# Kernel tuning notes

Measured on AMD Instinct MI355X. Metric: run time of the kernel, lower is better.

Reference implementation:

```python
import jax, jax.numpy as jnp
import numpy as np

N_USERS = 100000
EMBED_DIM = 64
MAX_NEIGHBORS = 50
BATCH = 16384


def setup_inputs() -> dict:
    key = jax.random.key(0)
    k1, k2, k3, k4 = jax.random.split(key, 4)
    nodes = jax.random.randint(k1, (BATCH,), 0, N_USERS, dtype=jnp.int64 if jax.config.read('jax_enable_x64') else jnp.int32)
    u_u = jax.random.randint(k2, (N_USERS, MAX_NEIGHBORS), 0, N_USERS, dtype=nodes.dtype)
    # integer-valued degrees in [0, MAX_NEIGHBORS], zeros included to exercise the inf-mask
    u_u_l = jax.random.randint(k3, (N_USERS, 1), 0, MAX_NEIGHBORS + 1).astype(jnp.float32)
    emb = jax.random.normal(k4, (N_USERS, EMBED_DIM), dtype=jnp.float32)
    return {"nodes": nodes, "u_u": u_u, "u_u_l": u_u_l, "emb": emb}


def reference(nodes, u_u, u_u_l, emb):
    tem_adj = u_u[nodes]                    # [B, K] neighbor ids
    e_u = emb[tem_adj]                      # [B, K, D] gathered neighbor embeddings
    N_a = u_u_l[nodes]                      # [B, 1] degree of center node
    N_b = u_u_l[tem_adj][..., 0]            # [B, K] degree of neighbors
    att_w = 1.0 / (jnp.sqrt(N_a) * jnp.sqrt(N_b))  # [B, K]
    att_w = jnp.where(jnp.isinf(att_w), 0.0, att_w)
    # bmm(e_u^T [B,D,K], att_w [B,K,1]) -> [B,D]
    embed_matrix = jnp.einsum('bkd,bk->bd', e_u, att_w)
    return embed_matrix
```

## Files before the change

### kernel.cpp

```cpp
#include <hip/hip_runtime.h>

#define D 64
#define K 50
#define GROUPS 8
#define KPAD 56
#define ITERS (KPAD / GROUPS)
#define RPB 8
#define THREADS 256

__global__ __launch_bounds__(THREADS)
void prep_q8(const float* __restrict__ emb, const float* __restrict__ deg,
             unsigned* __restrict__ emb8, float* __restrict__ rtab,
             float* __restrict__ wtab, int nuser)
{
    const int tid = blockIdx.x * THREADS + threadIdx.x;
    const int row = tid >> 4;
    const int sub = tid & 15;
    if (row >= nuser) return;

    const float4 f = ((const float4*)emb)[row * 16 + sub];
    float m = fmaxf(fmaxf(fabsf(f.x), fabsf(f.y)), fmaxf(fabsf(f.z), fabsf(f.w)));
    #pragma unroll
    for (int off = 1; off < 16; off <<= 1)
        m = fmaxf(m, __shfl_xor(m, off));
    const float inv = (m > 0.0f) ? 127.0f / m : 0.0f;
    const int q0 = (int)rintf(f.x * inv);
    const int q1 = (int)rintf(f.y * inv);
    const int q2 = (int)rintf(f.z * inv);
    const int q3 = (int)rintf(f.w * inv);
    const unsigned pk = (q0 & 0xFF) | ((q1 & 0xFF) << 8) |
                        ((q2 & 0xFF) << 16) | ((unsigned)(q3 & 0xFF) << 24);
    emb8[row * 16 + sub] = pk;
    if (sub == 0) {
        const float n = deg[row];
        const float r = (n > 0.0f) ? rsqrtf(n) : 0.0f;
        rtab[row] = r;
        wtab[row] = r * m * (1.0f / 127.0f);
    }
}

__device__ __forceinline__ float sb(unsigned v, int byte) {
    return (float)((int)(v << (24 - 8 * byte)) >> 24);
}

__global__ __launch_bounds__(THREADS)
void social_agg_q8(const int* __restrict__ nodes,
                   const int* __restrict__ u_u,
                   const float* __restrict__ rtab,
                   const float* __restrict__ wtab,
                   const unsigned* __restrict__ emb8,
                   float* __restrict__ out,
                   int batch)
{
    __shared__ uint2 nw[RPB][KPAD];
    const int base = blockIdx.x * RPB;

    for (int p = threadIdx.x; p < RPB * KPAD; p += THREADS) {
        const int r   = p / KPAD;
        const int k   = p - r * KPAD;
        const int row = base + r;
        int nb = 0; float w = 0.0f;
        if (row < batch && k < K) {
            const int node = nodes[row];
            nb = u_u[node * K + k];
            w  = rtab[node] * wtab[nb];
        }
        nw[r][k] = make_uint2((unsigned)nb, __float_as_uint(w));
    }
    __syncthreads();

    const int wave = threadIdx.x >> 6;
    const int lane = threadIdx.x & 63;
    const int g    = lane >> 3;
    const int sub  = lane & 7;
    const int r0   = wave * 2;
    const int row0 = base + r0;

    float a0[8] = {0,0,0,0,0,0,0,0};
    float a1[8] = {0,0,0,0,0,0,0,0};
    #pragma unroll
    for (int i = 0; i < ITERS; ++i) {
        const uint2 e0 = nw[r0][i * GROUPS + g];
        const uint2 e1 = nw[r0 + 1][i * GROUPS + g];
        const float w0 = __uint_as_float(e0.y);
        const float w1 = __uint_as_float(e1.y);
        const uint2 v0 = *(const uint2*)(emb8 + (size_t)e0.x * (D / 4) + sub * 2);
        const uint2 v1 = *(const uint2*)(emb8 + (size_t)e1.x * (D / 4) + sub * 2);
        a0[0] += w0 * sb(v0.x, 0); a0[1] += w0 * sb(v0.x, 1);
        a0[2] += w0 * sb(v0.x, 2); a0[3] += w0 * sb(v0.x, 3);
        a0[4] += w0 * sb(v0.y, 0); a0[5] += w0 * sb(v0.y, 1);
        a0[6] += w0 * sb(v0.y, 2); a0[7] += w0 * sb(v0.y, 3);
        a1[0] += w1 * sb(v1.x, 0); a1[1] += w1 * sb(v1.x, 1);
        a1[2] += w1 * sb(v1.x, 2); a1[3] += w1 * sb(v1.x, 3);
        a1[4] += w1 * sb(v1.y, 0); a1[5] += w1 * sb(v1.y, 1);
        a1[6] += w1 * sb(v1.y, 2); a1[7] += w1 * sb(v1.y, 3);
    }

    #pragma unroll
    for (int off = 8; off <= 32; off <<= 1) {
        #pragma unroll
        for (int j = 0; j < 8; ++j) { a0[j] += __shfl_xor(a0[j], off);
                                      a1[j] += __shfl_xor(a1[j], off); }
    }

    if (g == 0) {
        if (row0 < batch) {
            float* o = out + (size_t)row0 * D + sub * 8;
            *(float4*)(o)     = make_float4(a0[0], a0[1], a0[2], a0[3]);
            *(float4*)(o + 4) = make_float4(a0[4], a0[5], a0[6], a0[7]);
        }
        if (row0 + 1 < batch) {
            float* o = out + (size_t)(row0 + 1) * D + sub * 8;
            *(float4*)(o)     = make_float4(a1[0], a1[1], a1[2], a1[3]);
            *(float4*)(o + 4) = make_float4(a1[4], a1[5], a1[6], a1[7]);
        }
    }
}

__global__ __launch_bounds__(THREADS)
void social_agg_f32(const int* __restrict__ nodes,
                    const int* __restrict__ u_u,
                    const float* __restrict__ u_u_l,
                    const float* __restrict__ emb,
                    float* __restrict__ out,
                    int batch)
{
    __shared__ uint2 nw[4][52];
    const int base = blockIdx.x * 4;
    const int p = threadIdx.x;
    if (p < 4 * 52) {
        const int r = p / 52, k = p - r * 52, row = base + r;
        int nb = 0; float w = 0.0f;
        if (row < batch && k < K) {
            const int node = nodes[row];
            const float Na = u_u_l[node];
            nb = u_u[node * K + k];
            const float prod = Na * u_u_l[nb];
            w = (prod > 0.0f) ? rsqrtf(prod) : 0.0f;
        }
        nw[r][k] = make_uint2((unsigned)nb, __float_as_uint(w));
    }
    __syncthreads();
    const int wave = threadIdx.x >> 6, lane = threadIdx.x & 63;
    const int kk = lane >> 4, sub = lane & 15, row = base + wave;
    float4 acc = make_float4(0.f, 0.f, 0.f, 0.f);
    #pragma unroll
    for (int i = 0; i < 13; ++i) {
        const uint2 e = nw[wave][i * 4 + kk];
        const float wk = __uint_as_float(e.y);
        const float4 v = *(const float4*)(emb + (size_t)e.x * D + sub * 4);
        acc.x += wk * v.x; acc.y += wk * v.y; acc.z += wk * v.z; acc.w += wk * v.w;
    }
    #pragma unroll
    for (int off = 16; off <= 32; off <<= 1) {
        acc.x += __shfl_xor(acc.x, off);
        acc.y += __shfl_xor(acc.y, off);
        acc.z += __shfl_xor(acc.z, off);
        acc.w += __shfl_xor(acc.w, off);
    }
    if (row < batch && kk == 0)
        *(float4*)(out + (size_t)row * D + sub * 4) = acc;
}

extern "C" void kernel_launch(void* const* d_in, const int* in_sizes, int n_in,
                              void* d_out, int out_size, void* d_ws, size_t ws_size,
                              hipStream_t stream) {
    const int*   nodes = (const int*)d_in[0];
    const int*   u_u   = (const int*)d_in[1];
    const float* u_u_l = (const float*)d_in[2];
    const float* emb   = (const float*)d_in[3];
    float*       out   = (float*)d_out;

    const int batch = in_sizes[0];
    const int nuser = in_sizes[1] / K;

    const size_t emb8_bytes = (size_t)nuser * D;
    const size_t tab_bytes  = (size_t)nuser * 4;
    if (ws_size >= emb8_bytes + 2 * tab_bytes) {
        unsigned* emb8 = (unsigned*)d_ws;
        float*    rtab = (float*)((char*)d_ws + emb8_bytes);
        float*    wtab = (float*)((char*)d_ws + emb8_bytes + tab_bytes);
        const int pthreads = nuser * 16;
        const int pblocks  = (pthreads + THREADS - 1) / THREADS;
        prep_q8<<<pblocks, THREADS, 0, stream>>>(emb, u_u_l, emb8, rtab, wtab, nuser);
        const int blocks = (batch + RPB - 1) / RPB;
        social_agg_q8<<<blocks, THREADS, 0, stream>>>(nodes, u_u, rtab, wtab, emb8,
                                                      out, batch);
    } else {
        const int blocks = (batch + 3) / 4;
        social_agg_f32<<<blocks, THREADS, 0, stream>>>(nodes, u_u, u_u_l, emb,
                                                       out, batch);
    }
}
```

Before: 29.24 us.

## Interleave per-neighbor scale into quantized embedding rows, apply center factor at output

Each quantized embedding row now carries its per-row scale (neighbor rsqrt degree times quantization scale) in a padded 72-byte record. The main kernel reads the scale together with the int8 payload instead of doing a separate random gather into wtab during the staging phase. The center-node rsqrt factor is applied once per output row. Padding slots point to a zeroed sentinel row. This removes one dependent random gather per neighbor, but the row stride is no longer aligned to 64 bytes, so some rows span two cache lines.

```diff
diff --git a/kernel.cpp b/kernel.cpp
--- a/kernel.cpp
+++ b/kernel.cpp
@@ -7,15 +7,19 @@
 #define ITERS (KPAD / GROUPS)
 #define RPB 8
 #define THREADS 256
+#define ROW_BYTES 72
 
 __global__ __launch_bounds__(THREADS)
 void prep_q8(const float* __restrict__ emb, const float* __restrict__ deg,
-             unsigned* __restrict__ emb8, float* __restrict__ rtab,
-             float* __restrict__ wtab, int nuser)
+             char* __restrict__ tab, float* __restrict__ rtab, int nuser)
 {
     const int tid = blockIdx.x * THREADS + threadIdx.x;
     const int row = tid >> 4;
     const int sub = tid & 15;
+
+    if (blockIdx.x == 0 && threadIdx.x < ROW_BYTES / 4)
+        ((unsigned*)(tab + (size_t)nuser * ROW_BYTES))[threadIdx.x] = 0u;
+
     if (row >= nuser) return;
 
     const float4 f = ((const float4*)emb)[row * 16 + sub];
@@ -30,12 +34,13 @@
     const int q3 = (int)rintf(f.w * inv);
     const unsigned pk = (q0 & 0xFF) | ((q1 & 0xFF) << 8) |
                         ((q2 & 0xFF) << 16) | ((unsigned)(q3 & 0xFF) << 24);
-    emb8[row * 16 + sub] = pk;
+    char* rbase = tab + (size_t)row * ROW_BYTES;
+    *(unsigned*)(rbase + sub * 4) = pk;
     if (sub == 0) {
         const float n = deg[row];
         const float r = (n > 0.0f) ? rsqrtf(n) : 0.0f;
         rtab[row] = r;
-        wtab[row] = r * m * (1.0f / 127.0f);
+        *(float*)(rbase + 64) = r * m * (1.0f / 127.0f);
     }
 }
 
@@ -47,25 +52,26 @@
 void social_agg_q8(const int* __restrict__ nodes,
                    const int* __restrict__ u_u,
                    const float* __restrict__ rtab,
-                   const float* __restrict__ wtab,
-                   const unsigned* __restrict__ emb8,
+                   const char* __restrict__ tab,
                    float* __restrict__ out,
-                   int batch)
+                   int batch, int nuser)
 {
-    __shared__ uint2 nw[RPB][KPAD];
+    __shared__ unsigned ids[RPB][KPAD];
+    __shared__ float    cfac[RPB];
     const int base = blockIdx.x * RPB;
 
     for (int p = threadIdx.x; p < RPB * KPAD; p += THREADS) {
         const int r   = p / KPAD;
         const int k   = p - r * KPAD;
         const int row = base + r;
-        int nb = 0; float w = 0.0f;
-        if (row < batch && k < K) {
-            const int node = nodes[row];
-            nb = u_u[node * K + k];
-            w  = rtab[node] * wtab[nb];
-        }
-        nw[r][k] = make_uint2((unsigned)nb, __float_as_uint(w));
+        unsigned nb = (unsigned)nuser;
+        if (row < batch && k < K)
+            nb = (unsigned)u_u[nodes[row] * K + k];
+        ids[r][k] = nb;
+    }
+    if (threadIdx.x < RPB) {
+        const int row = base + threadIdx.x;
+        cfac[threadIdx.x] = (row < batch) ? rtab[nodes[row]] : 0.0f;
     }
     __syncthreads();
 
@@ -80,20 +86,22 @@
     float a1[8] = {0,0,0,0,0,0,0,0};
     #pragma unroll
     for (int i = 0; i < ITERS; ++i) {
-        const uint2 e0 = nw[r0][i * GROUPS + g];
-        const uint2 e1 = nw[r0 + 1][i * GROUPS + g];
-        const float w0 = __uint_as_float(e0.y);
-        const float w1 = __uint_as_float(e1.y);
-        const uint2 v0 = *(const uint2*)(emb8 + (size_t)e0.x * (D / 4) + sub * 2);
-        const uint2 v1 = *(const uint2*)(emb8 + (size_t)e1.x * (D / 4) + sub * 2);
-        a0[0] += w0 * sb(v0.x, 0); a0[1] += w0 * sb(v0.x, 1);
-        a0[2] += w0 * sb(v0.x, 2); a0[3] += w0 * sb(v0.x, 3);
-        a0[4] += w0 * sb(v0.y, 0); a0[5] += w0 * sb(v0.y, 1);
-        a0[6] += w0 * sb(v0.y, 2); a0[7] += w0 * sb(v0.y, 3);
-        a1[0] += w1 * sb(v1.x, 0); a1[1] += w1 * sb(v1.x, 1);
-        a1[2] += w1 * sb(v1.x, 2); a1[3] += w1 * sb(v1.x, 3);
-        a1[4] += w1 * sb(v1.y, 0); a1[5] += w1 * sb(v1.y, 1);
-        a1[6] += w1 * sb(v1.y, 2); a1[7] += w1 * sb(v1.y, 3);
+        const unsigned nb0 = ids[r0][i * GROUPS + g];
+        const unsigned nb1 = ids[r0 + 1][i * GROUPS + g];
+        const char* b0 = tab + (size_t)nb0 * ROW_BYTES;
+        const char* b1 = tab + (size_t)nb1 * ROW_BYTES;
+        const uint2 v0 = *(const uint2*)(b0 + sub * 8);
+        const uint2 v1 = *(const uint2*)(b1 + sub * 8);
+        const float f0 = *(const float*)(b0 + 64);
+        const float f1 = *(const float*)(b1 + 64);
+        a0[0] += f0 * sb(v0.x, 0); a0[1] += f0 * sb(v0.x, 1);
+        a0[2] += f0 * sb(v0.x, 2); a0[3] += f0 * sb(v0.x, 3);
+        a0[4] += f0 * sb(v0.y, 0); a0[5] += f0 * sb(v0.y, 1);
+        a0[6] += f0 * sb(v0.y, 2); a0[7] += f0 * sb(v0.y, 3);
+        a1[0] += f1 * sb(v1.x, 0); a1[1] += f1 * sb(v1.x, 1);
+        a1[2] += f1 * sb(v1.x, 2); a1[3] += f1 * sb(v1.x, 3);
+        a1[4] += f1 * sb(v1.y, 0); a1[5] += f1 * sb(v1.y, 1);
+        a1[6] += f1 * sb(v1.y, 2); a1[7] += f1 * sb(v1.y, 3);
     }
 
     #pragma unroll
@@ -105,14 +113,16 @@
 
     if (g == 0) {
         if (row0 < batch) {
+            const float c = cfac[r0];
             float* o = out + (size_t)row0 * D + sub * 8;
-            *(float4*)(o)     = make_float4(a0[0], a0[1], a0[2], a0[3]);
-            *(float4*)(o + 4) = make_float4(a0[4], a0[5], a0[6], a0[7]);
+            *(float4*)(o)     = make_float4(c*a0[0], c*a0[1], c*a0[2], c*a0[3]);
+            *(float4*)(o + 4) = make_float4(c*a0[4], c*a0[5], c*a0[6], c*a0[7]);
         }
         if (row0 + 1 < batch) {
+            const float c = cfac[r0 + 1];
             float* o = out + (size_t)(row0 + 1) * D + sub * 8;
-            *(float4*)(o)     = make_float4(a1[0], a1[1], a1[2], a1[3]);
-            *(float4*)(o + 4) = make_float4(a1[4], a1[5], a1[6], a1[7]);
+            *(float4*)(o)     = make_float4(c*a1[0], c*a1[1], c*a1[2], c*a1[3]);
+            *(float4*)(o + 4) = make_float4(c*a1[4], c*a1[5], c*a1[6], c*a1[7]);
         }
     }
 }
@@ -174,18 +184,17 @@
     const int batch = in_sizes[0];
     const int nuser = in_sizes[1] / K;
 
-    const size_t emb8_bytes = (size_t)nuser * D;
-    const size_t tab_bytes  = (size_t)nuser * 4;
-    if (ws_size >= emb8_bytes + 2 * tab_bytes) {
-        unsigned* emb8 = (unsigned*)d_ws;
-        float*    rtab = (float*)((char*)d_ws + emb8_bytes);
-        float*    wtab = (float*)((char*)d_ws + emb8_bytes + tab_bytes);
+    const size_t tab_bytes  = (size_t)(nuser + 1) * ROW_BYTES;
+    const size_t rtab_bytes = (size_t)nuser * 4;
+    if (ws_size >= tab_bytes + rtab_bytes) {
+        char*  tab  = (char*)d_ws;
+        float* rtab = (float*)((char*)d_ws + tab_bytes);
         const int pthreads = nuser * 16;
         const int pblocks  = (pthreads + THREADS - 1) / THREADS;
-        prep_q8<<<pblocks, THREADS, 0, stream>>>(emb, u_u_l, emb8, rtab, wtab, nuser);
+        prep_q8<<<pblocks, THREADS, 0, stream>>>(emb, u_u_l, tab, rtab, nuser);
         const int blocks = (batch + RPB - 1) / RPB;
-        social_agg_q8<<<blocks, THREADS, 0, stream>>>(nodes, u_u, rtab, wtab, emb8,
-                                                      out, batch);
+        social_agg_q8<<<blocks, THREADS, 0, stream>>>(nodes, u_u, rtab, tab,
+                                                      out, batch, nuser);
     } else {
         const int blocks = (batch + 3) / 4;
         social_agg_f32<<<blocks, THREADS, 0, stream>>>(nodes, u_u, u_u_l, emb,
```

New measurement: 29.15 us. No clear change (-0.3%).
